# Kernel tuning notes

Measured on AMD Instinct MI355X. Metric: run time of the kernel, lower is better.

Reference implementation:

```python
import jax, jax.numpy as jnp
import numpy as np

V, E, H = 32000, 512, 1024  # vocab, embedding_dim, hidden_dim
B, T = 16, 256


def _lstm_layer(x, mask, Wx, Wh, b):
    """Keras-semantics masked LSTM. x:[B,T,D], mask:[B,T] bool.
    Gate order i,f,g,o (Keras). Masked steps carry h,c (and output) forward."""
    Bx, Tx, _ = x.shape
    Hh = Wh.shape[0]
    xs = jnp.swapaxes(x, 0, 1)                       # [T,B,D]
    ms = jnp.swapaxes(mask, 0, 1)[..., None]         # [T,B,1]
    # hoist the input projection out of the scan (one big GEMM)
    xz = jnp.einsum('tbd,dh->tbh', xs, Wx) + b       # [T,B,4H]

    def step(carry, inp):
        h, c = carry
        zx, mt = inp
        z = zx + h @ Wh
        i, f, g, o = jnp.split(z, 4, axis=-1)
        i = jax.nn.sigmoid(i)
        f = jax.nn.sigmoid(f)
        g = jnp.tanh(g)
        o = jax.nn.sigmoid(o)
        c_new = f * c + i * g
        h_new = o * jnp.tanh(c_new)
        h2 = jnp.where(mt, h_new, h)
        c2 = jnp.where(mt, c_new, c)
        return (h2, c2), h2

    init = (jnp.zeros((Bx, Hh), x.dtype), jnp.zeros((Bx, Hh), x.dtype))
    _, ys = jax.lax.scan(step, init, (xz, ms))
    return jnp.swapaxes(ys, 0, 1)                    # [B,T,H]


def setup_inputs() -> dict:
    key = jax.random.key(0)
    ks = jax.random.split(key, 10)
    s = 0.02
    tokens = jax.random.randint(ks[0], (B, T), 0, V)
    emb = jax.random.normal(ks[1], (V, E), jnp.float32) * s
    Wx0 = jax.random.normal(ks[2], (E, 4 * H), jnp.float32) * s
    Wh0 = jax.random.normal(ks[3], (H, 4 * H), jnp.float32) * s
    b0 = jnp.zeros((4 * H,), jnp.float32).at[H:2 * H].set(1.0)  # unit_forget_bias
    Wx1 = jax.random.normal(ks[4], (H, 4 * H), jnp.float32) * s
    Wh1 = jax.random.normal(ks[5], (H, 4 * H), jnp.float32) * s
    b1 = jnp.zeros((4 * H,), jnp.float32).at[H:2 * H].set(1.0)
    Wout = jax.random.normal(ks[6], (H, V), jnp.float32) * s
    bout = jnp.zeros((V,), jnp.float32)
    return {"tokens": tokens, "emb": emb, "Wx0": Wx0, "Wh0": Wh0, "b0": b0,
            "Wx1": Wx1, "Wh1": Wh1, "b1": b1, "Wout": Wout, "bout": bout}


def reference(tokens, emb, Wx0, Wh0, b0, Wx1, Wh1, b1, Wout, bout):
    mask = tokens != 0                               # mask_zero=True
    x = emb[tokens]                                  # [B,T,E]
    x = _lstm_layer(x, mask, Wx0, Wh0, b0)
    x = _lstm_layer(x, mask, Wx1, Wh1, b1)
    logits = x @ Wout + bout                         # [B,T,V]
    fm = mask[..., None].astype(logits.dtype)
    onehot0 = jnp.zeros((V,), logits.dtype).at[0].set(1.0)  # tf.eye(V)[0]
    return logits * fm + onehot0 * (1.0 - fm)
```

## Files before the change

### kernel.cpp

```cpp
#include <hip/hip_runtime.h>

#define B_ 16
#define T_ 256
#define E_ 512
#define H_ 1024
#define V_ 32000
#define HX16 (H_ * 16)

typedef float f32x4 __attribute__((ext_vector_type(4)));
typedef short short8 __attribute__((ext_vector_type(8)));

typedef __attribute__((address_space(1))) const void gas_t;
typedef __attribute__((address_space(3))) void las_t;

__device__ __forceinline__ unsigned short f2bf(float x) {
    unsigned int u = __float_as_uint(x);
    u += 0x7FFF + ((u >> 16) & 1);
    return (unsigned short)(u >> 16);
}
__device__ __forceinline__ float bf2f(unsigned short b) {
    return __uint_as_float(((unsigned int)b) << 16);
}
__device__ __forceinline__ float fsig(float x) {
    return __fdividef(1.f, 1.f + __expf(-x));
}
__device__ __forceinline__ float ftanh(float x) {
    float xc = fminf(fmaxf(x, -15.f), 15.f);
    float e  = __expf(-2.f * xc);
    return __fdividef(1.f - e, 1.f + e);
}

__global__ __launch_bounds__(256)
void gather_cvt_k(const int* __restrict__ tokens, const float* __restrict__ emb,
                  unsigned short* __restrict__ Ah, unsigned short* __restrict__ Al)
{
    int i  = blockIdx.x * 256 + threadIdx.x;
    int bt = i >> 7;
    int e4 = i & 127;
    float4 v = ((const float4*)(emb + (size_t)tokens[bt] * E_))[e4];
    ushort4 h, l;
    h.x = f2bf(v.x); l.x = f2bf(v.x - bf2f(h.x));
    h.y = f2bf(v.y); l.y = f2bf(v.y - bf2f(h.y));
    h.z = f2bf(v.z); l.z = f2bf(v.z - bf2f(h.z));
    h.w = f2bf(v.w); l.w = f2bf(v.w - bf2f(h.w));
    ((ushort4*)Ah)[i] = h;
    ((ushort4*)Al)[i] = l;
}

__global__ __launch_bounds__(256)
void cvt_k(const float* __restrict__ A, unsigned short* __restrict__ Ah,
           unsigned short* __restrict__ Al)
{
    int i = blockIdx.x * 256 + threadIdx.x;
    float4 v = ((const float4*)A)[i];
    ushort4 h, l;
    h.x = f2bf(v.x); l.x = f2bf(v.x - bf2f(h.x));
    h.y = f2bf(v.y); l.y = f2bf(v.y - bf2f(h.y));
    h.z = f2bf(v.z); l.z = f2bf(v.z - bf2f(h.z));
    h.w = f2bf(v.w); l.w = f2bf(v.w - bf2f(h.w));
    ((ushort4*)Ah)[i] = h;
    ((ushort4*)Al)[i] = l;
}

__global__ __launch_bounds__(256)
void twz_k(const float* __restrict__ W, unsigned short* __restrict__ Bh,
           unsigned short* __restrict__ Bl, int Kd, int Nfull, int n0)
{
    __shared__ float tile[32][33];
    int t  = threadIdx.x;
    int tx = t & 31, ty = t >> 5;
    int nb = blockIdx.x * 32, kb = blockIdx.y * 32;
    #pragma unroll
    for (int i = 0; i < 4; ++i)
        tile[ty + i * 8][tx] = W[(size_t)(kb + ty + i * 8) * Nfull + n0 + nb + tx];
    __syncthreads();
    #pragma unroll
    for (int i = 0; i < 4; ++i) {
        float v = tile[tx][ty + i * 8];
        unsigned short h = f2bf(v), l = f2bf(v - bf2f(h));
        size_t o = (size_t)(nb + ty + i * 8) * Kd + kb + tx;
        Bh[o] = h; Bl[o] = l;
    }
}

template<int DO_MASK>
__global__ __launch_bounds__(256)
void mgemm_k(const unsigned short* __restrict__ Ah, const unsigned short* __restrict__ Al,
             const unsigned short* __restrict__ Bh, const unsigned short* __restrict__ Bl,
             const float* __restrict__ bias, float* __restrict__ C,
             const int* __restrict__ tokens, int K, int ldc, int n0)
{
    __shared__ unsigned short LDSS[4][128 * 64];

    const int tid  = threadIdx.x;
    const int nwg = gridDim.x * gridDim.y;
    int lin = blockIdx.y * gridDim.x + blockIdx.x;
    lin = (lin & 7) * (nwg >> 3) + (lin >> 3);
    const int bm   = (lin / gridDim.x) * 128;
    const int bn   = (lin % gridDim.x) * 128;
    const int w    = tid >> 6, lane = tid & 63;
    const int wm   = (w >> 1) * 64, wn = (w & 1) * 64;
    const int l15  = lane & 15, lhi = lane >> 4;

    const unsigned short* gp = (w == 0) ? Ah : (w == 1) ? Al : (w == 2) ? Bh : Bl;
    const int rb = (w < 2) ? bm : bn;
    const int srow = lane >> 3;
    const int scol = (lane & 7) ^ srow;
    unsigned short* lbase = &LDSS[w][0];

    f32x4 acc[4][4];
    #pragma unroll
    for (int mi = 0; mi < 4; ++mi)
        #pragma unroll
        for (int ni = 0; ni < 4; ++ni) {
            f32x4 z = {0.f, 0.f, 0.f, 0.f};
            acc[mi][ni] = z;
        }

    for (int kt = 0; kt < K; kt += 64) {
        #pragma unroll
        for (int c = 0; c < 16; ++c) {
            const unsigned short* src =
                gp + (size_t)(rb + c * 8 + srow) * K + kt + scol * 8;
            __builtin_amdgcn_global_load_lds((gas_t*)src,
                                             (las_t*)(lbase + c * 512), 16, 0, 0);
        }
        __syncthreads();
        #pragma unroll
        for (int ks = 0; ks < 2; ++ks) {
            short8 ah[4], al[4], bh[4], bl[4];
            const int s = ks * 4 + lhi;
            #pragma unroll
            for (int mi = 0; mi < 4; ++mi) {
                int m = wm + mi * 16 + l15;
                int off = m * 64 + ((s ^ (m & 7)) * 8);
                ah[mi] = *(const short8*)(&LDSS[0][off]);
                al[mi] = *(const short8*)(&LDSS[1][off]);
            }
            #pragma unroll
            for (int ni = 0; ni < 4; ++ni) {
                int n = wn + ni * 16 + l15;
                int off = n * 64 + ((s ^ (n & 7)) * 8);
                bh[ni] = *(const short8*)(&LDSS[2][off]);
                bl[ni] = *(const short8*)(&LDSS[3][off]);
            }
            #pragma unroll
            for (int mi = 0; mi < 4; ++mi)
                #pragma unroll
                for (int ni = 0; ni < 4; ++ni) {
                    acc[mi][ni] = __builtin_amdgcn_mfma_f32_16x16x32_bf16(
                        ah[mi], bh[ni], acc[mi][ni], 0, 0, 0);
                    acc[mi][ni] = __builtin_amdgcn_mfma_f32_16x16x32_bf16(
                        ah[mi], bl[ni], acc[mi][ni], 0, 0, 0);
                    acc[mi][ni] = __builtin_amdgcn_mfma_f32_16x16x32_bf16(
                        al[mi], bh[ni], acc[mi][ni], 0, 0, 0);
                }
        }
        __syncthreads();
    }

    #pragma unroll
    for (int mi = 0; mi < 4; ++mi) {
        #pragma unroll
        for (int r = 0; r < 4; ++r) {
            int row = bm + wm + mi * 16 + lhi * 4 + r;
            bool msk = true;
            if (DO_MASK) msk = (tokens[row] != 0);
            #pragma unroll
            for (int ni = 0; ni < 4; ++ni) {
                int col = bn + wn + ni * 16 + l15;
                float v = acc[mi][ni][r] + bias[n0 + col];
                if (DO_MASK && !msk) v = ((n0 + col) == 0) ? 1.f : 0.f;
                C[(size_t)row * ldc + n0 + col] = v;
            }
        }
    }
}

__global__ __launch_bounds__(256)
void wprep_k(const float* __restrict__ Wh, uint4* __restrict__ WhF,
             unsigned* __restrict__ flags, int nrst)
{
    int flat = blockIdx.x * 256 + threadIdx.x;
    if (flat < nrst) flags[flat] = 0;
    int l  = flat & 63;
    int kf = (flat >> 6) & 3;
    int ct = (flat >> 8) & 3;
    int w  = (flat >> 10) & 7;
    int bx = flat >> 13;
    int k0  = w * 128 + kf * 32 + 8 * (l >> 4);
    int col = ct * H_ + bx * 16 + (l & 15);
    unsigned short hi[8], lo[8];
    #pragma unroll
    for (int j = 0; j < 8; ++j) {
        float v = Wh[(size_t)(k0 + j) * (4 * H_) + col];
        hi[j] = f2bf(v); lo[j] = f2bf(v - bf2f(hi[j]));
    }
    size_t base = ((((size_t)bx * 8 + w) * 4 + ct) * 4 + kf) * 2;
    WhF[(base + 0) * 64 + l] = *(uint4*)hi;
    WhF[(base + 1) * 64 + l] = *(uint4*)lo;
}

#define HLOAD_MFMA(HT_BASE, TIDX)                                             \
    do {                                                                      \
        const unsigned* hTp_ = (HT_BASE) + (size_t)(TIDX) * HX16;             \
        unsigned hd[4][8];                                                    \
        _Pragma("unroll")                                                     \
        for (int kf = 0; kf < 4; ++kf) {                                      \
            const int k0 = w * 128 + kf * 32 + 8 * lhi;                       \
            _Pragma("unroll")                                                 \
            for (int j = 0; j < 8; ++j) {                                     \
                const unsigned* ap = hTp_ + (k0 + j) * 16 + l15;              \
                asm volatile("global_load_dword %0, %1, off sc0 sc1"          \
                             : "=&v"(hd[kf][j]) : "v"(ap));                   \
            }                                                                 \
        }                                                                     \
        asm volatile("s_waitcnt vmcnt(0)" ::: "memory");                      \
        __builtin_amdgcn_sched_barrier(0);                                    \
        f32x4 a0 = {0.f,0.f,0.f,0.f}, a1 = a0, a2 = a0, a3 = a0;              \
        _Pragma("unroll")                                                     \
        for (int kf = 0; kf < 4; ++kf) {                                      \
            unsigned short hh[8], hl[8];                                      \
            _Pragma("unroll")                                                 \
            for (int j = 0; j < 8; ++j) {                                     \
                unsigned d = hd[kf][j];                                       \
                hh[j] = (unsigned short)(d >> 16);                            \
                hl[j] = (unsigned short)(d & 0xFFFFu);                        \
            }                                                                 \
            short8 ah = *(short8*)hh, al = *(short8*)hl;                      \
            a0 = __builtin_amdgcn_mfma_f32_16x16x32_bf16(ah, Bhi[0][kf], a0, 0,0,0); \
            a0 = __builtin_amdgcn_mfma_f32_16x16x32_bf16(ah, Blo[0][kf], a0, 0,0,0); \
            a0 = __builtin_amdgcn_mfma_f32_16x16x32_bf16(al, Bhi[0][kf], a0, 0,0,0); \
            a1 = __builtin_amdgcn_mfma_f32_16x16x32_bf16(ah, Bhi[1][kf], a1, 0,0,0); \
            a1 = __builtin_amdgcn_mfma_f32_16x16x32_bf16(ah, Blo[1][kf], a1, 0,0,0); \
            a1 = __builtin_amdgcn_mfma_f32_16x16x32_bf16(al, Bhi[1][kf], a1, 0,0,0); \
            a2 = __builtin_amdgcn_mfma_f32_16x16x32_bf16(ah, Bhi[2][kf], a2, 0,0,0); \
            a2 = __builtin_amdgcn_mfma_f32_16x16x32_bf16(ah, Blo[2][kf], a2, 0,0,0); \
            a2 = __builtin_amdgcn_mfma_f32_16x16x32_bf16(al, Bhi[2][kf], a2, 0,0,0); \
            a3 = __builtin_amdgcn_mfma_f32_16x16x32_bf16(ah, Bhi[3][kf], a3, 0,0,0); \
            a3 = __builtin_amdgcn_mfma_f32_16x16x32_bf16(ah, Blo[3][kf], a3, 0,0,0); \
            a3 = __builtin_amdgcn_mfma_f32_16x16x32_bf16(al, Bhi[3][kf], a3, 0,0,0); \
        }                                                                     \
        _Pragma("unroll")                                                     \
        for (int r = 0; r < 4; ++r) {                                         \
            Rs2[r * 2048 + (0 * 8 + w) * 64 + l] = a0[r];                     \
            Rs2[r * 2048 + (1 * 8 + w) * 64 + l] = a1[r];                     \
            Rs2[r * 2048 + (2 * 8 + w) * 64 + l] = a2[r];                     \
            Rs2[r * 2048 + (3 * 8 + w) * 64 + l] = a3[r];                     \
        }                                                                     \
    } while (0)

__global__ __launch_bounds__(512, 1)
void lstm_fused_k(const float* __restrict__ xz0,
                  const uint4* __restrict__ WhF0,
                  const uint4* __restrict__ WxF1,
                  const uint4* __restrict__ WhF1,
                  const float* __restrict__ b1v,
                  float* __restrict__ xz1,
                  unsigned* __restrict__ hT0,
                  unsigned* __restrict__ hT1,
                  float* __restrict__ h1seq,
                  const int* __restrict__ tokens,
                  unsigned* __restrict__ flags)
{
    __shared__ float Rs2[4 * 2048];

    unsigned* flagsL0  = flags;
    unsigned* flagsP   = flags + 64;
    unsigned* flagsL1  = flags + 128;
    unsigned* flagsL0b = flags + 192;

    const int tid  = threadIdx.x;
    const int role = blockIdx.x >> 6;
    const int bx   = blockIdx.x & 63;
    const int w    = tid >> 6;
    const int l    = tid & 63;
    const int l15  = l & 15, lhi = l >> 4;
    const int u    = bx * 16 + l15;
    const int bl   = lhi * 4 + w;
    const size_t bt_base = (size_t)bl * T_;

    short8 Bhi[4][4], Blo[4][4];
    {
        const uint4* wimg = (role == 0) ? WhF0 : (role == 1) ? WxF1 : WhF1;
        const uint4* p = wimg + (((size_t)bx * 8 + w) * 32) * 64;
        #pragma unroll
        for (int ct = 0; ct < 4; ++ct)
            #pragma unroll
            for (int kf = 0; kf < 4; ++kf) {
                uint4 hv = p[((ct * 4 + kf) * 2 + 0) * 64 + l];
                uint4 lv = p[((ct * 4 + kf) * 2 + 1) * 64 + l];
                Bhi[ct][kf] = *(short8*)&hv;
                Blo[ct][kf] = *(short8*)&lv;
            }
    }
    #pragma unroll
    for (int ct = 0; ct < 4; ++ct)
        #pragma unroll
        for (int kf = 0; kf < 4; ++kf) {
            asm volatile("" : "+v"(Bhi[ct][kf]));
            asm volatile("" : "+v"(Blo[ct][kf]));
        }

    if (role == 0) {
        float c1 = 0.f, h1 = 0.f;
        for (int t = 0; t < T_; ++t) {
            float xzr[4];
            int tok = 0;
            if (w < 4) {
                size_t bt = bt_base + t;
                #pragma unroll
                for (int ct = 0; ct < 4; ++ct)
                    xzr[ct] = xz0[bt * 4096 + (size_t)ct * H_ + u];
                tok = tokens[bt];
            }
            if (t > 0) HLOAD_MFMA(hT0, t - 1);
            __syncthreads();

            if (w < 4) {
                float z[4];
                #pragma unroll
                for (int ct = 0; ct < 4; ++ct) {
                    float s = 0.f;
                    if (t > 0) {
                        #pragma unroll
                        for (int w2 = 0; w2 < 8; ++w2)
                            s += Rs2[w * 2048 + (ct * 8 + w2) * 64 + l];
                    }
                    z[ct] = s + xzr[ct];
                }
                float i_ = fsig(z[0]);
                float f_ = fsig(z[1]);
                float g_ = ftanh(z[2]);
                float o_ = fsig(z[3]);
                float c_new = f_ * c1 + i_ * g_;
                float h_new = o_ * ftanh(c_new);
                bool  m  = (tok != 0);
                float h2 = m ? h_new : h1;
                c1 = m ? c_new : c1;
                h1 = h2;
                unsigned short hh = f2bf(h2);
                unsigned short hl = f2bf(h2 - bf2f(hh));
                unsigned pack = ((unsigned)hh << 16) | hl;
                __hip_atomic_store(&hT0[(size_t)t * HX16 + u * 16 + bl], pack,
                                   __ATOMIC_RELAXED, __HIP_MEMORY_SCOPE_AGENT);
                asm volatile("s_waitcnt vmcnt(0)" ::: "memory");
            }
            __syncthreads();

            if (w == 0) {
                if (l == 0) {
                    __hip_atomic_store(&flagsL0[bx], (unsigned)(t + 1),
                                       __ATOMIC_RELAXED, __HIP_MEMORY_SCOPE_AGENT);
                    __hip_atomic_store(&flagsL0b[bx], (unsigned)(t + 1),
                                       __ATOMIC_RELAXED, __HIP_MEMORY_SCOPE_AGENT);
                }
                if (t + 1 < T_) {
                    const unsigned tgt = (unsigned)(t + 1);
                    while (true) {
                        unsigned fv = __hip_atomic_load(&flagsL0[l],
                            __ATOMIC_RELAXED, __HIP_MEMORY_SCOPE_AGENT);
                        if (__all(fv >= tgt)) break;
                        __builtin_amdgcn_s_sleep(1);
                    }
                }
            }
            __syncthreads();
        }
    } else if (role == 1) {
        float b1r[4];
        if (w < 4) {
            #pragma unroll
            for (int ct = 0; ct < 4; ++ct) b1r[ct] = b1v[ct * H_ + u];
        }
        for (int t = 0; t < T_; ++t) {
            if (w == 0) {
                const unsigned tgt = (unsigned)(t + 1);
                while (true) {
                    unsigned fv = __hip_atomic_load(&flagsL0b[l],
                        __ATOMIC_RELAXED, __HIP_MEMORY_SCOPE_AGENT);
                    if (__all(fv >= tgt)) break;
                    __builtin_amdgcn_s_sleep(1);
                }
            }
            __syncthreads();

            HLOAD_MFMA(hT0, t);
            __syncthreads();

            if (w < 4) {
                size_t bt = bt_base + t;
                #pragma unroll
                for (int ct = 0; ct < 4; ++ct) {
                    float s = 0.f;
                    #pragma unroll
                    for (int w2 = 0; w2 < 8; ++w2)
                        s += Rs2[w * 2048 + (ct * 8 + w2) * 64 + l];
                    float z = s + b1r[ct];
                    const float* ap = xz1 + bt * 4096 + (size_t)ct * H_ + u;
                    asm volatile("global_store_dword %0, %1, off sc0 sc1"
                                 :: "v"(ap), "v"(z) : "memory");
                }
                asm volatile("s_waitcnt vmcnt(0)" ::: "memory");
            }
            __syncthreads();
            if (tid == 0)
                __hip_atomic_store(&flagsP[bx], (unsigned)(t + 1),
                                   __ATOMIC_RELAXED, __HIP_MEMORY_SCOPE_AGENT);
        }
    } else {
        float c1 = 0.f, h1 = 0.f;
        for (int t = 0; t < T_; ++t) {
            if (w == 0) {
                const unsigned tp = (unsigned)(t + 1);
                while (true) {
                    unsigned f1 = __hip_atomic_load(&flagsP[l],
                        __ATOMIC_RELAXED, __HIP_MEMORY_SCOPE_AGENT);
                    unsigned f2 = __hip_atomic_load(&flagsL1[l],
                        __ATOMIC_RELAXED, __HIP_MEMORY_SCOPE_AGENT);
                    bool ok = (f1 >= tp) && (t == 0 || f2 >= (unsigned)t);
                    if (__all(ok)) break;
                    __builtin_amdgcn_s_sleep(1);
                }
            }
            __syncthreads();

            float xzr[4];
            int tok = 0;
            if (w < 4) {
                size_t bt = bt_base + t;
                #pragma unroll
                for (int ct = 0; ct < 4; ++ct) {
                    const float* ap = xz1 + bt * 4096 + (size_t)ct * H_ + u;
                    asm volatile("global_load_dword %0, %1, off sc0 sc1"
                                 : "=&v"(xzr[ct]) : "v"(ap));
                }
                tok = tokens[bt];
            }
            if (t > 0) HLOAD_MFMA(hT1, t - 1);
            __syncthreads();

            if (w < 4) {
                asm volatile("s_waitcnt vmcnt(0)" ::: "memory");
                __builtin_amdgcn_sched_barrier(0);
                float z[4];
                #pragma unroll
                for (int ct = 0; ct < 4; ++ct) {
                    float s = 0.f;
                    if (t > 0) {
                        #pragma unroll
                        for (int w2 = 0; w2 < 8; ++w2)
                            s += Rs2[w * 2048 + (ct * 8 + w2) * 64 + l];
                    }
                    z[ct] = s + xzr[ct];
                }
                float i_ = fsig(z[0]);
                float f_ = fsig(z[1]);
                float g_ = ftanh(z[2]);
                float o_ = fsig(z[3]);
                float c_new = f_ * c1 + i_ * g_;
                float h_new = o_ * ftanh(c_new);
                bool  m  = (tok != 0);
                float h2 = m ? h_new : h1;
                c1 = m ? c_new : c1;
                h1 = h2;
                size_t bt = bt_base + t;
                unsigned short hh = f2bf(h2);
                unsigned short hl = f2bf(h2 - bf2f(hh));
                unsigned pack = ((unsigned)hh << 16) | hl;
                __hip_atomic_store(&hT1[(size_t)t * HX16 + u * 16 + bl], pack,
                                   __ATOMIC_RELAXED, __HIP_MEMORY_SCOPE_AGENT);
                asm volatile("s_waitcnt vmcnt(0)" ::: "memory");
                h1seq[bt * H_ + u] = h2;
            }
            __syncthreads();
            if (tid == 0)
                __hip_atomic_store(&flagsL1[bx], (unsigned)(t + 1),
                                   __ATOMIC_RELAXED, __HIP_MEMORY_SCOPE_AGENT);
        }
    }
}

extern "C" void kernel_launch(void* const* d_in, const int* in_sizes, int n_in,
                              void* d_out, int out_size, void* d_ws, size_t ws_size,
                              hipStream_t stream)
{
    const int*   tokens = (const int*)d_in[0];
    const float* emb    = (const float*)d_in[1];
    const float* Wx0    = (const float*)d_in[2];
    const float* Wh0    = (const float*)d_in[3];
    const float* b0     = (const float*)d_in[4];
    const float* Wx1    = (const float*)d_in[5];
    const float* Wh1    = (const float*)d_in[6];
    const float* b1     = (const float*)d_in[7];
    const float* Wout   = (const float*)d_in[8];
    const float* bout   = (const float*)d_in[9];
    float* out = (float*)d_out;

    unsigned short* wsu = (unsigned short*)d_ws;
    const size_t BPL = (size_t)16000 * 1024;
    const size_t AP  = (size_t)4096 * 1024;
    unsigned short* Bh  = wsu;
    unsigned short* Bl  = wsu + BPL;
    unsigned short* Ahp = wsu + 2 * BPL;
    unsigned short* Alp = Ahp + AP;
    unsigned* flags = (unsigned*)(wsu + 2 * BPL + 2 * AP);

    float* f    = (float*)d_out;
    float* xz0  = f;
    float* xz1  = xz0 + (size_t)4096 * 4096;
    float* WhF0 = xz1 + (size_t)4096 * 4096;
    float* WxF1 = WhF0 + (size_t)1024 * 4096;
    float* WhF1 = WxF1 + (size_t)1024 * 4096;
    unsigned* hT0 = (unsigned*)(WhF1 + (size_t)1024 * 4096);
    unsigned* hT1 = hT0 + (size_t)T_ * HX16;
    float* h1s  = (float*)(hT1 + (size_t)T_ * HX16);

    dim3 blk(256);

    gather_cvt_k<<<2048, blk, 0, stream>>>(tokens, emb, Ahp, Alp);
    twz_k<<<dim3(128, 16), blk, 0, stream>>>(Wx0, Bh, Bl, 512, 4096, 0);
    mgemm_k<0><<<dim3(32, 32), blk, 0, stream>>>(Ahp, Alp, Bh, Bl, b0, xz0,
                                                 nullptr, 512, 4096, 0);
    wprep_k<<<2048, blk, 0, stream>>>(Wh0, (uint4*)WhF0, flags, 64);
    wprep_k<<<2048, blk, 0, stream>>>(Wx1, (uint4*)WxF1, flags + 64, 64);
    wprep_k<<<2048, blk, 0, stream>>>(Wh1, (uint4*)WhF1, flags + 128, 128);
    {
        void* args[] = {(void*)&xz0, (void*)&WhF0, (void*)&WxF1, (void*)&WhF1,
                        (void*)&b1, (void*)&xz1, (void*)&hT0, (void*)&hT1,
                        (void*)&h1s, (void*)&tokens, (void*)&flags};
        hipLaunchCooperativeKernel((void*)lstm_fused_k, dim3(192), dim3(512),
                                   args, 0, stream);
    }
    cvt_k<<<4096, blk, 0, stream>>>(h1s, Ahp, Alp);
    twz_k<<<dim3(500, 32), blk, 0, stream>>>(Wout, Bh, Bl, 1024, 32000, 0);
    mgemm_k<1><<<dim3(125, 32), blk, 0, stream>>>(Ahp, Alp, Bh, Bl, bout, out,
                                                  tokens, 1024, 32000, 0);
    twz_k<<<dim3(500, 32), blk, 0, stream>>>(Wout, Bh, Bl, 1024, 32000, 16000);
    mgemm_k<1><<<dim3(125, 32), blk, 0, stream>>>(Ahp, Alp, Bh, Bl, bout, out,
                                                  tokens, 1024, 32000, 16000);
}
```

Measured before the change: 2.472 ms.

## Replace flag-based inter-block sync with sentinel-polling on data buffers

Removes the per-step flag arrays and spin-waits between blocks in the cooperative LSTM kernel. Consumers now poll the h and xz1 data buffers directly, which are prefilled with a 0xFFFFFFFF sentinel, and retry until no sentinel remains. This drops the store-wait-flag round trip on every timestep. The layer-1 output is also written straight to the bf16 hi/lo GEMM operand buffers, so the separate conversion kernel goes away. In exchange it adds a sentinel fill pass over xz1 and hT0/hT1, and it relies on real values never matching the sentinel.

```diff
diff --git a/kernel.cpp b/kernel.cpp
--- a/kernel.cpp
+++ b/kernel.cpp
@@ -6,6 +6,7 @@
 #define H_ 1024
 #define V_ 32000
 #define HX16 (H_ * 16)
+#define SENT 0xFFFFFFFFu
 
 typedef float f32x4 __attribute__((ext_vector_type(4)));
 typedef short short8 __attribute__((ext_vector_type(8)));
@@ -38,21 +39,6 @@
     int bt = i >> 7;
     int e4 = i & 127;
     float4 v = ((const float4*)(emb + (size_t)tokens[bt] * E_))[e4];
-    ushort4 h, l;
-    h.x = f2bf(v.x); l.x = f2bf(v.x - bf2f(h.x));
-    h.y = f2bf(v.y); l.y = f2bf(v.y - bf2f(h.y));
-    h.z = f2bf(v.z); l.z = f2bf(v.z - bf2f(h.z));
-    h.w = f2bf(v.w); l.w = f2bf(v.w - bf2f(h.w));
-    ((ushort4*)Ah)[i] = h;
-    ((ushort4*)Al)[i] = l;
-}
-
-__global__ __launch_bounds__(256)
-void cvt_k(const float* __restrict__ A, unsigned short* __restrict__ Ah,
-           unsigned short* __restrict__ Al)
-{
-    int i = blockIdx.x * 256 + threadIdx.x;
-    float4 v = ((const float4*)A)[i];
     ushort4 h, l;
     h.x = f2bf(v.x); l.x = f2bf(v.x - bf2f(h.x));
     h.y = f2bf(v.y); l.y = f2bf(v.y - bf2f(h.y));
@@ -178,11 +164,9 @@
 }
 
 __global__ __launch_bounds__(256)
-void wprep_k(const float* __restrict__ Wh, uint4* __restrict__ WhF,
-             unsigned* __restrict__ flags, int nrst)
+void wprep_k(const float* __restrict__ Wh, uint4* __restrict__ WhF)
 {
     int flat = blockIdx.x * 256 + threadIdx.x;
-    if (flat < nrst) flags[flat] = 0;
     int l  = flat & 63;
     int kf = (flat >> 6) & 3;
     int ct = (flat >> 8) & 3;
@@ -201,22 +185,17 @@
     WhF[(base + 1) * 64 + l] = *(uint4*)lo;
 }
 
-#define HLOAD_MFMA(HT_BASE, TIDX)                                             \
+__global__ __launch_bounds__(256)
+void sfill_k(uint4* __restrict__ p, unsigned n4)
+{
+    uint4 s = {SENT, SENT, SENT, SENT};
+    for (size_t i = (size_t)blockIdx.x * 256 + threadIdx.x; i < n4;
+         i += (size_t)gridDim.x * 256)
+        p[i] = s;
+}
+
+#define MFMA_FROM_HD()                                                        \
     do {                                                                      \
-        const unsigned* hTp_ = (HT_BASE) + (size_t)(TIDX) * HX16;             \
-        unsigned hd[4][8];                                                    \
-        _Pragma("unroll")                                                     \
-        for (int kf = 0; kf < 4; ++kf) {                                      \
-            const int k0 = w * 128 + kf * 32 + 8 * lhi;                       \
-            _Pragma("unroll")                                                 \
-            for (int j = 0; j < 8; ++j) {                                     \
-                const unsigned* ap = hTp_ + (k0 + j) * 16 + l15;              \
-                asm volatile("global_load_dword %0, %1, off sc0 sc1"          \
-                             : "=&v"(hd[kf][j]) : "v"(ap));                   \
-            }                                                                 \
-        }                                                                     \
-        asm volatile("s_waitcnt vmcnt(0)" ::: "memory");                      \
-        __builtin_amdgcn_sched_barrier(0);                                    \
         f32x4 a0 = {0.f,0.f,0.f,0.f}, a1 = a0, a2 = a0, a3 = a0;              \
         _Pragma("unroll")                                                     \
         for (int kf = 0; kf < 4; ++kf) {                                      \
@@ -250,6 +229,30 @@
         }                                                                     \
     } while (0)
 
+#define ISSUE_H(HT_BASE, TIDX)                                                \
+    do {                                                                      \
+        const unsigned* hTp_ = (HT_BASE) + (size_t)(TIDX) * HX16;             \
+        _Pragma("unroll")                                                     \
+        for (int kf = 0; kf < 4; ++kf) {                                      \
+            const int k0 = w * 128 + kf * 32 + 8 * lhi;                       \
+            _Pragma("unroll")                                                 \
+            for (int j = 0; j < 8; ++j) {                                     \
+                const unsigned* ap = hTp_ + (k0 + j) * 16 + l15;              \
+                asm volatile("global_load_dword %0, %1, off sc0 sc1"          \
+                             : "=&v"(hd[kf][j]) : "v"(ap));                   \
+            }                                                                 \
+        }                                                                     \
+    } while (0)
+
+#define HD_BAD(BADV)                                                          \
+    do {                                                                      \
+        _Pragma("unroll")                                                     \
+        for (int kf = 0; kf < 4; ++kf)                                        \
+            _Pragma("unroll")                                                 \
+            for (int j = 0; j < 8; ++j)                                       \
+                (BADV) |= (hd[kf][j] == SENT);                                \
+    } while (0)
+
 __global__ __launch_bounds__(512, 1)
 void lstm_fused_k(const float* __restrict__ xz0,
                   const uint4* __restrict__ WhF0,
@@ -259,16 +262,11 @@
                   float* __restrict__ xz1,
                   unsigned* __restrict__ hT0,
                   unsigned* __restrict__ hT1,
-                  float* __restrict__ h1seq,
-                  const int* __restrict__ tokens,
-                  unsigned* __restrict__ flags)
+                  unsigned short* __restrict__ Ahp,
+                  unsigned short* __restrict__ Alp,
+                  const int* __restrict__ tokens)
 {
     __shared__ float Rs2[4 * 2048];
-
-    unsigned* flagsL0  = flags;
-    unsigned* flagsP   = flags + 64;
-    unsigned* flagsL1  = flags + 128;
-    unsigned* flagsL0b = flags + 192;
 
     const int tid  = threadIdx.x;
     const int role = blockIdx.x >> 6;
@@ -303,7 +301,7 @@
         }
 
     if (role == 0) {
-        float c1 = 0.f, h1 = 0.f;
+        float c1 = 0.f, h1v = 0.f;
         for (int t = 0; t < T_; ++t) {
             float xzr[4];
             int tok = 0;
@@ -314,7 +312,19 @@
                     xzr[ct] = xz0[bt * 4096 + (size_t)ct * H_ + u];
                 tok = tokens[bt];
             }
-            if (t > 0) HLOAD_MFMA(hT0, t - 1);
+            if (t > 0) {
+                unsigned hd[4][8];
+                while (true) {
+                    ISSUE_H(hT0, t - 1);
+                    asm volatile("s_waitcnt vmcnt(0)" ::: "memory");
+                    __builtin_amdgcn_sched_barrier(0);
+                    bool bad = false;
+                    HD_BAD(bad);
+                    if (!__any(bad)) break;
+                    __builtin_amdgcn_s_sleep(2);
+                }
+                MFMA_FROM_HD();
+            }
             __syncthreads();
 
             if (w < 4) {
@@ -336,34 +346,14 @@
                 float c_new = f_ * c1 + i_ * g_;
                 float h_new = o_ * ftanh(c_new);
                 bool  m  = (tok != 0);
-                float h2 = m ? h_new : h1;
-                c1 = m ? c_new : c1;
-                h1 = h2;
+                float h2 = m ? h_new : h1v;
+                c1  = m ? c_new : c1;
+                h1v = h2;
                 unsigned short hh = f2bf(h2);
                 unsigned short hl = f2bf(h2 - bf2f(hh));
                 unsigned pack = ((unsigned)hh << 16) | hl;
                 __hip_atomic_store(&hT0[(size_t)t * HX16 + u * 16 + bl], pack,
                                    __ATOMIC_RELAXED, __HIP_MEMORY_SCOPE_AGENT);
-                asm volatile("s_waitcnt vmcnt(0)" ::: "memory");
-            }
-            __syncthreads();
-
-            if (w == 0) {
-                if (l == 0) {
-                    __hip_atomic_store(&flagsL0[bx], (unsigned)(t + 1),
-                                       __ATOMIC_RELAXED, __HIP_MEMORY_SCOPE_AGENT);
-                    __hip_atomic_store(&flagsL0b[bx], (unsigned)(t + 1),
-                                       __ATOMIC_RELAXED, __HIP_MEMORY_SCOPE_AGENT);
-                }
-                if (t + 1 < T_) {
-                    const unsigned tgt = (unsigned)(t + 1);
-                    while (true) {
-                        unsigned fv = __hip_atomic_load(&flagsL0[l],
-                            __ATOMIC_RELAXED, __HIP_MEMORY_SCOPE_AGENT);
-                        if (__all(fv >= tgt)) break;
-                        __builtin_amdgcn_s_sleep(1);
-                    }
-                }
             }
             __syncthreads();
         }
@@ -374,18 +364,19 @@
             for (int ct = 0; ct < 4; ++ct) b1r[ct] = b1v[ct * H_ + u];
         }
         for (int t = 0; t < T_; ++t) {
-            if (w == 0) {
-                const unsigned tgt = (unsigned)(t + 1);
+            {
+                unsigned hd[4][8];
                 while (true) {
-                    unsigned fv = __hip_atomic_load(&flagsL0b[l],
-                        __ATOMIC_RELAXED, __HIP_MEMORY_SCOPE_AGENT);
-                    if (__all(fv >= tgt)) break;
-                    __builtin_amdgcn_s_sleep(1);
-                }
-            }
-            __syncthreads();
-
-            HLOAD_MFMA(hT0, t);
+                    ISSUE_H(hT0, t);
+                    asm volatile("s_waitcnt vmcnt(0)" ::: "memory");
+                    __builtin_amdgcn_sched_barrier(0);
+                    bool bad = false;
+                    HD_BAD(bad);
+                    if (!__any(bad)) break;
+                    __builtin_amdgcn_s_sleep(2);
+                }
+                MFMA_FROM_HD();
+            }
             __syncthreads();
 
             if (w < 4) {
@@ -401,48 +392,42 @@
                     asm volatile("global_store_dword %0, %1, off sc0 sc1"
                                  :: "v"(ap), "v"(z) : "memory");
                 }
-                asm volatile("s_waitcnt vmcnt(0)" ::: "memory");
             }
             __syncthreads();
-            if (tid == 0)
-                __hip_atomic_store(&flagsP[bx], (unsigned)(t + 1),
-                                   __ATOMIC_RELAXED, __HIP_MEMORY_SCOPE_AGENT);
         }
     } else {
-        float c1 = 0.f, h1 = 0.f;
+        float c1 = 0.f, h1v = 0.f;
         for (int t = 0; t < T_; ++t) {
-            if (w == 0) {
-                const unsigned tp = (unsigned)(t + 1);
-                while (true) {
-                    unsigned f1 = __hip_atomic_load(&flagsP[l],
-                        __ATOMIC_RELAXED, __HIP_MEMORY_SCOPE_AGENT);
-                    unsigned f2 = __hip_atomic_load(&flagsL1[l],
-                        __ATOMIC_RELAXED, __HIP_MEMORY_SCOPE_AGENT);
-                    bool ok = (f1 >= tp) && (t == 0 || f2 >= (unsigned)t);
-                    if (__all(ok)) break;
-                    __builtin_amdgcn_s_sleep(1);
-                }
-            }
-            __syncthreads();
-
-            float xzr[4];
+            unsigned hd[4][8];
+            unsigned xzu[4];
             int tok = 0;
-            if (w < 4) {
-                size_t bt = bt_base + t;
-                #pragma unroll
-                for (int ct = 0; ct < 4; ++ct) {
-                    const float* ap = xz1 + bt * 4096 + (size_t)ct * H_ + u;
-                    asm volatile("global_load_dword %0, %1, off sc0 sc1"
-                                 : "=&v"(xzr[ct]) : "v"(ap));
-                }
-                tok = tokens[bt];
-            }
-            if (t > 0) HLOAD_MFMA(hT1, t - 1);
-            __syncthreads();
-
-            if (w < 4) {
+            size_t bt = bt_base + t;
+            if (w < 4) tok = tokens[bt];
+            while (true) {
+                if (w < 4) {
+                    #pragma unroll
+                    for (int ct = 0; ct < 4; ++ct) {
+                        const float* ap = xz1 + bt * 4096 + (size_t)ct * H_ + u;
+                        asm volatile("global_load_dword %0, %1, off sc0 sc1"
+                                     : "=&v"(xzu[ct]) : "v"(ap));
+                    }
+                }
+                if (t > 0) ISSUE_H(hT1, t - 1);
                 asm volatile("s_waitcnt vmcnt(0)" ::: "memory");
                 __builtin_amdgcn_sched_barrier(0);
+                bool bad = false;
+                if (w < 4) {
+                    #pragma unroll
+                    for (int ct = 0; ct < 4; ++ct) bad |= (xzu[ct] == SENT);
+                }
+                if (t > 0) HD_BAD(bad);
+                if (!__any(bad)) break;
+                __builtin_amdgcn_s_sleep(2);
+            }
+            if (t > 0) MFMA_FROM_HD();
+            __syncthreads();
+
+            if (w < 4) {
                 float z[4];
                 #pragma unroll
                 for (int ct = 0; ct < 4; ++ct) {
@@ -452,7 +437,7 @@
                         for (int w2 = 0; w2 < 8; ++w2)
                             s += Rs2[w * 2048 + (ct * 8 + w2) * 64 + l];
                     }
-                    z[ct] = s + xzr[ct];
+                    z[ct] = s + __uint_as_float(xzu[ct]);
                 }
                 float i_ = fsig(z[0]);
                 float f_ = fsig(z[1]);
@@ -461,22 +446,18 @@
                 float c_new = f_ * c1 + i_ * g_;
                 float h_new = o_ * ftanh(c_new);
                 bool  m  = (tok != 0);
-                float h2 = m ? h_new : h1;
-                c1 = m ? c_new : c1;
-                h1 = h2;
-                size_t bt = bt_base + t;
+                float h2 = m ? h_new : h1v;
+                c1  = m ? c_new : c1;
+                h1v = h2;
                 unsigned short hh = f2bf(h2);
                 unsigned short hl = f2bf(h2 - bf2f(hh));
                 unsigned pack = ((unsigned)hh << 16) | hl;
                 __hip_atomic_store(&hT1[(size_t)t * HX16 + u * 16 + bl], pack,
                                    __ATOMIC_RELAXED, __HIP_MEMORY_SCOPE_AGENT);
-                asm volatile("s_waitcnt vmcnt(0)" ::: "memory");
-                h1seq[bt * H_ + u] = h2;
+                Ahp[bt * (size_t)H_ + u] = hh;
+                Alp[bt * (size_t)H_ + u] = hl;
             }
             __syncthreads();
-            if (tid == 0)
-                __hip_atomic_store(&flagsL1[bx], (unsigned)(t + 1),
-                                   __ATOMIC_RELAXED, __HIP_MEMORY_SCOPE_AGENT);
         }
     }
 }
@@ -504,17 +485,15 @@
     unsigned short* Bl  = wsu + BPL;
     unsigned short* Ahp = wsu + 2 * BPL;
     unsigned short* Alp = Ahp + AP;
-    unsigned* flags = (unsigned*)(wsu + 2 * BPL + 2 * AP);
 
     float* f    = (float*)d_out;
     float* xz0  = f;
-    float* xz1  = xz0 + (size_t)4096 * 4096;
-    float* WhF0 = xz1 + (size_t)4096 * 4096;
+    float* WhF0 = xz0 + (size_t)4096 * 4096;
     float* WxF1 = WhF0 + (size_t)1024 * 4096;
     float* WhF1 = WxF1 + (size_t)1024 * 4096;
-    unsigned* hT0 = (unsigned*)(WhF1 + (size_t)1024 * 4096);
+    float* xz1  = WhF1 + (size_t)1024 * 4096;
+    unsigned* hT0 = (unsigned*)(xz1 + (size_t)4096 * 4096);
     unsigned* hT1 = hT0 + (size_t)T_ * HX16;
-    float* h1s  = (float*)(hT1 + (size_t)T_ * HX16);
 
     dim3 blk(256);
 
@@ -522,17 +501,17 @@
     twz_k<<<dim3(128, 16), blk, 0, stream>>>(Wx0, Bh, Bl, 512, 4096, 0);
     mgemm_k<0><<<dim3(32, 32), blk, 0, stream>>>(Ahp, Alp, Bh, Bl, b0, xz0,
                                                  nullptr, 512, 4096, 0);
-    wprep_k<<<2048, blk, 0, stream>>>(Wh0, (uint4*)WhF0, flags, 64);
-    wprep_k<<<2048, blk, 0, stream>>>(Wx1, (uint4*)WxF1, flags + 64, 64);
-    wprep_k<<<2048, blk, 0, stream>>>(Wh1, (uint4*)WhF1, flags + 128, 128);
+    wprep_k<<<2048, blk, 0, stream>>>(Wh0, (uint4*)WhF0);
+    wprep_k<<<2048, blk, 0, stream>>>(Wx1, (uint4*)WxF1);
+    wprep_k<<<2048, blk, 0, stream>>>(Wh1, (uint4*)WhF1);
+    sfill_k<<<4096, blk, 0, stream>>>((uint4*)xz1, 6291456u);
     {
         void* args[] = {(void*)&xz0, (void*)&WhF0, (void*)&WxF1, (void*)&WhF1,
                         (void*)&b1, (void*)&xz1, (void*)&hT0, (void*)&hT1,
-                        (void*)&h1s, (void*)&tokens, (void*)&flags};
+                        (void*)&Ahp, (void*)&Alp, (void*)&tokens};
         hipLaunchCooperativeKernel((void*)lstm_fused_k, dim3(192), dim3(512),
                                    args, 0, stream);
     }
-    cvt_k<<<4096, blk, 0, stream>>>(h1s, Ahp, Alp);
     twz_k<<<dim3(500, 32), blk, 0, stream>>>(Wout, Bh, Bl, 1024, 32000, 0);
     mgemm_k<1><<<dim3(125, 32), blk, 0, stream>>>(Ahp, Alp, Bh, Bl, bout, out,
                                                   tokens, 1024, 32000, 0);
```

New measurement: 2.339 ms. -5.4%, faster.
